# Optimization experiments

Measured on AMD Instinct MI355X. Metric: run time of the kernel, lower is better.

## Reference

```python
import jax, jax.numpy as jnp
import numpy as np

EPS = 1e-5  # torch BatchNorm1d default eps


def _bn(x, gamma, beta):
    # training-mode BatchNorm1d over the point dimension
    m = jnp.mean(x, axis=0)
    v = jnp.var(x, axis=0)
    return (x - m) * jax.lax.rsqrt(v + EPS) * gamma + beta


def setup_inputs() -> dict:
    key = jax.random.key(0)
    ks = jax.random.split(key, 8)
    N, D = 1000000, 9
    G, V = 32, 32768  # 32^3 voxel grid; with 1M points all voxels occupied w.h.p.
    feats = jax.random.normal(ks[0], (N, D), dtype=jnp.float32)
    coords = jax.random.randint(ks[1], (N, 3), 0, G, dtype=jnp.int32)

    def lin(k, fan_in, fan_out):
        kw, kb = jax.random.split(k)
        s = 1.0 / np.sqrt(fan_in)
        W = jax.random.uniform(kw, (fan_in, fan_out), jnp.float32, -s, s)
        b = jax.random.uniform(kb, (fan_out,), jnp.float32, -s, s)
        return W, b

    W1, b1 = lin(ks[2], 9, 64)
    W2, b2 = lin(ks[3], 64, 128)
    W3, b3 = lin(ks[4], 128, 256)
    W4, b4 = lin(ks[5], 256, 256)
    return {
        'feats': feats, 'coords': coords, 'num_voxels': V,
        'g0': jnp.ones((9,), jnp.float32), 'be0': jnp.zeros((9,), jnp.float32),
        'W1': W1, 'b1': b1,
        'g1': jnp.ones((64,), jnp.float32), 'be1': jnp.zeros((64,), jnp.float32),
        'W2': W2, 'b2': b2,
        'g2': jnp.ones((128,), jnp.float32), 'be2': jnp.zeros((128,), jnp.float32),
        'W3': W3, 'b3': b3,
        'g3': jnp.ones((256,), jnp.float32), 'be3': jnp.zeros((256,), jnp.float32),
        'W4': W4, 'b4': b4,
    }


def _mlp(x, g0, be0, W1, b1, g1, be1, W2, b2, g2, be2, W3, b3, g3, be3, W4, b4):
    x = _bn(x, g0, be0)
    x = jax.nn.relu(_bn(x @ W1 + b1, g1, be1))
    x = jax.nn.relu(_bn(x @ W2 + b2, g2, be2))
    x = jax.nn.relu(_bn(x @ W3 + b3, g3, be3))
    return x @ W4 + b4


def reference(feats, coords, num_voxels, g0, be0, W1, b1, g1, be1, W2, b2,
              g2, be2, W3, b3, g3, be3, W4, b4):
    # NOTE: the torch module shuffles points first; unique(dim=0) is sorted and
    # scatter_max is permutation-invariant, so the shuffle does not affect output.
    unq_coords, unq_inv = jnp.unique(
        coords, axis=0, return_inverse=True, size=num_voxels, fill_value=0)
    unq_inv = unq_inv.reshape(-1)
    unq_coords = unq_coords.astype(jnp.int64)
    h = _mlp(feats, g0, be0, W1, b1, g1, be1, W2, b2, g2, be2, W3, b3, g3, be3, W4, b4)
    pooled = jax.ops.segment_max(h, unq_inv, num_segments=num_voxels)  # [V, 256]
    return pooled, unq_coords
```

## Files before the change

### kernel.cpp

```cpp
#include <hip/hip_runtime.h>
#include <math.h>

#define TPB 256
#define PT 64
#define NVOX 32768
#define VB 8
#define BN_EPS 1e-5f

typedef short s16x8 __attribute__((ext_vector_type(8)));
typedef short s16x4 __attribute__((ext_vector_type(4)));
typedef float f32x4 __attribute__((ext_vector_type(4)));

#define P0_OFF     0u
#define P1_OFF     256u
#define P2_OFF     (P1_OFF + 64u*128u*4u)
#define P3_OFF     (P2_OFF + 64u*256u*4u)
#define PAR_END    (P3_OFF + 64u*512u*4u)
#define A0_OFF     229632u
#define C0_OFF     229888u
#define A1_OFF     230144u
#define C1_OFF     230400u
#define A2_OFF     230656u
#define C2_OFF     231680u
#define A3_OFF     232704u
#define C3_OFF     233728u
#define HIST_OFF   234752u
#define BASE_OFF   (HIST_OFF + 131072u)
#define CURS_OFF   (BASE_OFF + 131328u)
#define PERM_OFF   (CURS_OFF + 131072u)
#define WT1_OFF    (PERM_OFF + 4000000u)
#define WT2_OFF    (WT1_OFF + 4096u)
#define WT3_OFF    (WT2_OFF + 16384u)
#define WT4_OFF    (WT3_OFF + 65536u)
#define X_OFF      4845568u

#define ACT0_OFF 0
#define ACT1_OFF 4096
#define ACT2_OFF 12288
#define ACT3_OFF 32768
#define H4_OFF   0
#define SMEM_S1  4096
#define SMEM_S2  12288
#define SMEM_S3  28672
#define SMEM_S4  65536

__device__ __forceinline__ unsigned short f2bf(float f) {
    unsigned u = __float_as_uint(f);
    u += 0x7FFFu + ((u >> 16) & 1u);
    return (unsigned short)(u >> 16);
}
__device__ __forceinline__ float bf2f(unsigned short h) {
    return __uint_as_float(((unsigned)h) << 16);
}

template<int ROWB>
__device__ __forceinline__ int swz(int row, int b) {
    constexpr int M = (ROWB >= 128) ? 7 : ((ROWB >= 64) ? 3 : 1);
    return row * ROWB + (b ^ ((row & M) << 4));
}

__device__ __forceinline__ s16x4 bn_relu_pack(f32x4 acc, f32x4 av, f32x4 cv) {
    s16x4 pk;
#pragma unroll
    for (int r = 0; r < 4; ++r) pk[r] = (short)f2bf(fmaxf(fmaf(acc[r], av[r], cv[r]), 0.f));
    return pk;
}

template<int NOUT>
__device__ __forceinline__ void stats_red(f32x4 ps, f32x4 pq, int ch, float* prow) {
#pragma unroll
    for (int m = 1; m <= 8; m <<= 1) {
#pragma unroll
        for (int r = 0; r < 4; ++r) { ps[r] += __shfl_xor(ps[r], m); pq[r] += __shfl_xor(pq[r], m); }
    }
    if ((threadIdx.x & 15) == 0) {
#pragma unroll
        for (int r = 0; r < 4; ++r) {
            atomicAdd(&prow[ch + r], ps[r]);
            atomicAdd(&prow[NOUT + ch + r], pq[r]);
        }
    }
}

__global__ void k_prepw(const float* __restrict__ W1, const float* __restrict__ W2,
                        const float* __restrict__ W3, const float* __restrict__ W4,
                        unsigned short* __restrict__ wt1, unsigned short* __restrict__ wt2,
                        unsigned short* __restrict__ wt3, unsigned short* __restrict__ wt4) {
    for (int i = blockIdx.x * blockDim.x + threadIdx.x; i < 108544;
         i += gridDim.x * blockDim.x) {
        if (i < 2048) {
            int n = i >> 5, k = i & 31;
            wt1[i] = (k < 9) ? f2bf(W1[k * 64 + n]) : (unsigned short)0;
        } else if (i < 10240) {
            int j = i - 2048; int n = j >> 6, k = j & 63;
            wt2[j] = f2bf(W2[k * 128 + n]);
        } else if (i < 43008) {
            int j = i - 10240; int n = j >> 7, k = j & 127;
            wt3[j] = f2bf(W3[k * 256 + n]);
        } else {
            int j = i - 43008; int n = j >> 8, k = j & 255;
            wt4[j] = f2bf(W4[k * 256 + n]);
        }
    }
}

__global__ void k_hist(const int* __restrict__ coords, int N, unsigned* __restrict__ hist) {
    for (int i = blockIdx.x * blockDim.x + threadIdx.x; i < N;
         i += gridDim.x * blockDim.x) {
        int v = (coords[3 * i] << 10) | (coords[3 * i + 1] << 5) | coords[3 * i + 2];
        atomicAdd(&hist[v], 1u);
    }
}

__global__ void k_scan(const unsigned* __restrict__ hist, int* __restrict__ base,
                       unsigned* __restrict__ cursor, int N) {
    __shared__ unsigned part[1024];
    const int t = threadIdx.x;
    unsigned sum = 0;
    for (int j = 0; j < 32; ++j) sum += hist[t * 32 + j];
    part[t] = sum;
    __syncthreads();
    for (int d = 1; d < 1024; d <<= 1) {
        unsigned v = (t >= d) ? part[t - d] : 0u;
        __syncthreads();
        part[t] += v;
        __syncthreads();
    }
    unsigned run = part[t] - sum;
    for (int j = 0; j < 32; ++j) {
        unsigned h = hist[t * 32 + j];
        base[t * 32 + j] = (int)run;
        cursor[t * 32 + j] = run;
        run += h;
    }
    if (t == 1023) base[32768] = (int)run;
}

__global__ void k_scatter(const int* __restrict__ coords, int N,
                          unsigned* __restrict__ cursor, int* __restrict__ perm) {
    for (int i = blockIdx.x * blockDim.x + threadIdx.x; i < N;
         i += gridDim.x * blockDim.x) {
        int v = (coords[3 * i] << 10) | (coords[3 * i + 1] << 5) | coords[3 * i + 2];
        unsigned pos = atomicAdd(&cursor[v], 1u);
        perm[pos] = i;
    }
}

__global__ void k_stats0(const float* __restrict__ feats, int N, float* __restrict__ p0) {
    __shared__ float s[9], q[9];
    if (threadIdx.x < 9) { s[threadIdx.x] = 0.f; q[threadIdx.x] = 0.f; }
    __syncthreads();
    float ls[9] = {0}, lq[9] = {0};
    for (size_t i = (size_t)blockIdx.x * blockDim.x + threadIdx.x; i < (size_t)N;
         i += (size_t)gridDim.x * blockDim.x) {
        const float* r = feats + i * 9;
#pragma unroll
        for (int c = 0; c < 9; ++c) { float v = r[c]; ls[c] += v; lq[c] += v * v; }
    }
#pragma unroll
    for (int c = 0; c < 9; ++c) { atomicAdd(&s[c], ls[c]); atomicAdd(&q[c], lq[c]); }
    __syncthreads();
    if (threadIdx.x < 9) {
        atomicAdd(&p0[threadIdx.x], s[threadIdx.x]);
        atomicAdd(&p0[9 + threadIdx.x], q[threadIdx.x]);
    }
}

__global__ void k_fin(const float* __restrict__ part, int nparts, int C,
                      const float* __restrict__ g, const float* __restrict__ be,
                      const float* __restrict__ bias,
                      float* __restrict__ A, float* __restrict__ Cc, float n) {
    int c = threadIdx.x;
    if (c >= C) return;
    float s = 0.f, q = 0.f;
    for (int r = 0; r < nparts; ++r) { s += part[r * 2 * C + c]; q += part[r * 2 * C + C + c]; }
    float m = s / n;
    float v = q / n - m * m;
    float a = g[c] * rsqrtf(v + BN_EPS);
    float cc = be[c] - m * a;
    A[c] = a;
    Cc[c] = bias ? fmaf(a, bias[c], cc) : cc;
}

__global__ void k_coords(float* __restrict__ outc) {
    int v = blockIdx.x * blockDim.x + threadIdx.x;
    if (v < NVOX) {
        outc[3 * v + 0] = (float)(v >> 10);
        outc[3 * v + 1] = (float)((v >> 5) & 31);
        outc[3 * v + 2] = (float)(v & 31);
    }
}


__global__ __launch_bounds__(256, 4) void k_pass1(
    const float* __restrict__ feats, const int* __restrict__ perm,
    const unsigned short* __restrict__ wt1,
    const float* __restrict__ A0, const float* __restrict__ C0,
    const float* __restrict__ b1,
    unsigned short* __restrict__ Xg, float* __restrict__ p1,
    int N, int nt) {
    __shared__ char Xl[8192];
    const int tid = threadIdx.x;
    const int w = tid >> 6, lane = tid & 63, g = lane >> 4, lq = lane & 15;
    const int chb = w * 16;
    const s16x8 a1 = *(const s16x8*)(wt1 + (chb + lq) * 32 + g * 8);
    const int ch = chb + g * 4;
    const f32x4 bv = *(const f32x4*)(b1 + ch);
    float* prow = p1 + (blockIdx.x & 63) * 128;

    for (int t = blockIdx.x; t < nt; t += gridDim.x) {
        const int t0 = t * 128;
        *(f32x4*)(Xl + tid * 32) = (f32x4){0.f, 0.f, 0.f, 0.f};
        *(f32x4*)(Xl + tid * 32 + 16) = (f32x4){0.f, 0.f, 0.f, 0.f};
        __syncthreads();
        for (int idx = tid; idx < 128 * 9; idx += 256) {
            const int p = idx / 9, c = idx - p * 9;
            const int gp = t0 + p;
            if (gp < N) {
                const int src = perm[gp];
                float v = fmaf(feats[(size_t)src * 9 + c], A0[c], C0[c]);
                *(unsigned short*)(Xl + swz<64>(p, c * 2)) = f2bf(v);
            }
        }
        __syncthreads();
        {
            const int row = tid >> 1, c = (tid & 1) * 16;
            *(s16x8*)(Xg + (size_t)(t0 + row) * 16 + c / 2) =
                *(const s16x8*)(Xl + swz<64>(row, c));
        }
        f32x4 acc[8];
#pragma unroll
        for (int ct = 0; ct < 8; ++ct) acc[ct] = (f32x4){0.f, 0.f, 0.f, 0.f};
#pragma unroll
        for (int ct = 0; ct < 8; ++ct) {
            const s16x8 b = *(const s16x8*)(Xl + swz<64>(ct * 16 + lq, g * 16));
            acc[ct] = __builtin_amdgcn_mfma_f32_16x16x32_bf16(a1, b, acc[ct], 0, 0, 0);
        }
        f32x4 ps = (f32x4){0.f,0.f,0.f,0.f}, pq = (f32x4){0.f,0.f,0.f,0.f};
#pragma unroll
        for (int ct = 0; ct < 8; ++ct) {
            const bool valid = (t0 + ct * 16 + lq) < N;
#pragma unroll
            for (int r = 0; r < 4; ++r) {
                const float h = valid ? (acc[ct][r] + bv[r]) : 0.f;
                ps[r] += h; pq[r] += h * h;
            }
        }
        stats_red<64>(ps, pq, ch, prow);
        __syncthreads();
    }
}

__global__ __launch_bounds__(256, 2) void k_pass2(
    const unsigned short* __restrict__ Xg,
    const unsigned short* __restrict__ wt1, const unsigned short* __restrict__ wt2,
    const float* __restrict__ A1, const float* __restrict__ C1,
    const float* __restrict__ b2,
    float* __restrict__ p2, int N, int nt) {
    __shared__ char smem[40960];
    char* Wt2l = smem;
    char* Xl   = smem + 16384;
    char* act1 = smem + 24576;
    const int tid = threadIdx.x;
    const int w = tid >> 6, lane = tid & 63, g = lane >> 4, lq = lane & 15;
    const int chb1 = w * 16, chb2 = w * 32;

    for (int i = tid; i < 1024; i += 256) {
        const int row = i >> 3, c = (i & 7) * 16;
        *(s16x8*)(Wt2l + swz<128>(row, c)) = *(const s16x8*)(wt2 + row * 64 + c / 2);
    }
    const s16x8 a1 = *(const s16x8*)(wt1 + (chb1 + lq) * 32 + g * 8);
    const int ch1 = chb1 + g * 4;
    const f32x4 av1 = *(const f32x4*)(A1 + ch1);
    const f32x4 cv1 = *(const f32x4*)(C1 + ch1);
    f32x4 bv2[2];
#pragma unroll
    for (int mt = 0; mt < 2; ++mt) bv2[mt] = *(const f32x4*)(b2 + chb2 + mt * 16 + g * 4);
    float* prow = p2 + (blockIdx.x & 63) * 256;

    for (int t = blockIdx.x; t < nt; t += gridDim.x) {
        const int t0 = t * 128;
        for (int i = tid; i < 512; i += 256) {
            const int row = i >> 2, c = (i & 3) * 16;
            s16x8 v = (s16x8){0,0,0,0,0,0,0,0};
            if (c < 32) v = *(const s16x8*)(Xg + (size_t)(t0 + row) * 16 + c / 2);
            *(s16x8*)(Xl + swz<64>(row, c)) = v;
        }
        __syncthreads();
        f32x4 acc1[8];
#pragma unroll
        for (int ct = 0; ct < 8; ++ct) acc1[ct] = (f32x4){0.f,0.f,0.f,0.f};
#pragma unroll
        for (int ct = 0; ct < 8; ++ct) {
            const s16x8 b = *(const s16x8*)(Xl + swz<64>(ct * 16 + lq, g * 16));
            acc1[ct] = __builtin_amdgcn_mfma_f32_16x16x32_bf16(a1, b, acc1[ct], 0, 0, 0);
        }
#pragma unroll
        for (int ct = 0; ct < 8; ++ct)
            *(s16x4*)(act1 + swz<128>(ct * 16 + lq, ch1 * 2)) = bn_relu_pack(acc1[ct], av1, cv1);
        __syncthreads();
        f32x4 acc2[2][8];
#pragma unroll
        for (int mt = 0; mt < 2; ++mt)
#pragma unroll
            for (int ct = 0; ct < 8; ++ct) acc2[mt][ct] = (f32x4){0.f,0.f,0.f,0.f};
#pragma unroll
        for (int kc = 0; kc < 2; ++kc) {
            s16x8 a[2];
#pragma unroll
            for (int mt = 0; mt < 2; ++mt)
                a[mt] = *(const s16x8*)(Wt2l + swz<128>(chb2 + mt * 16 + lq, kc * 64 + g * 16));
#pragma unroll
            for (int ct = 0; ct < 8; ++ct) {
                const s16x8 b = *(const s16x8*)(act1 + swz<128>(ct * 16 + lq, kc * 64 + g * 16));
#pragma unroll
                for (int mt = 0; mt < 2; ++mt)
                    acc2[mt][ct] = __builtin_amdgcn_mfma_f32_16x16x32_bf16(a[mt], b, acc2[mt][ct], 0, 0, 0);
            }
        }
#pragma unroll
        for (int mt = 0; mt < 2; ++mt) {
            f32x4 ps = (f32x4){0.f,0.f,0.f,0.f}, pq = (f32x4){0.f,0.f,0.f,0.f};
#pragma unroll
            for (int ct = 0; ct < 8; ++ct) {
                const bool valid = (t0 + ct * 16 + lq) < N;
#pragma unroll
                for (int r = 0; r < 4; ++r) {
                    const float h = valid ? (acc2[mt][ct][r] + bv2[mt][r]) : 0.f;
                    ps[r] += h; pq[r] += h * h;
                }
            }
            stats_red<128>(ps, pq, chb2 + mt * 16 + g * 4, prow);
        }
        __syncthreads();
    }
}

__global__ __launch_bounds__(512, 2) void k_pass3(
    const unsigned short* __restrict__ Xg,
    const unsigned short* __restrict__ wt1, const unsigned short* __restrict__ wt2,
    const unsigned short* __restrict__ wt3,
    const float* __restrict__ A1, const float* __restrict__ C1,
    const float* __restrict__ A2, const float* __restrict__ C2,
    const float* __restrict__ b3,
    float* __restrict__ p3, int N, int nt) {
    extern __shared__ char smem[];
    char* Wt2l = smem;
    char* act1 = smem + 16384;
    char* act2 = smem + 32768;
    char* Xl   = smem + 32768;
    const int tid = threadIdx.x;
    const int w = tid >> 6, lane = tid & 63, g = lane >> 4, lq = lane & 15;
    const int wm = w >> 1, wn = w & 1;
    const int chb1 = wm * 16, chb2 = w * 16, chb3 = w * 32;

    for (int i = tid; i < 1024; i += 512) {
        const int row = i >> 3, c = (i & 7) * 16;
        *(s16x8*)(Wt2l + swz<128>(row, c)) = *(const s16x8*)(wt2 + row * 64 + c / 2);
    }
    s16x8 w3[2][4];
#pragma unroll
    for (int mt = 0; mt < 2; ++mt)
#pragma unroll
        for (int kc = 0; kc < 4; ++kc)
            w3[mt][kc] = *(const s16x8*)(wt3 + (size_t)(chb3 + mt * 16 + lq) * 128 + kc * 32 + g * 8);
    const s16x8 a1 = *(const s16x8*)(wt1 + (chb1 + lq) * 32 + g * 8);
    const int ch1 = chb1 + g * 4, ch2 = chb2 + g * 4;
    const f32x4 av1 = *(const f32x4*)(A1 + ch1);
    const f32x4 cv1 = *(const f32x4*)(C1 + ch1);
    const f32x4 av2 = *(const f32x4*)(A2 + ch2);
    const f32x4 cv2 = *(const f32x4*)(C2 + ch2);
    f32x4 bv3[2];
#pragma unroll
    for (int mt = 0; mt < 2; ++mt) bv3[mt] = *(const f32x4*)(b3 + chb3 + mt * 16 + g * 4);
    float* prow = p3 + (blockIdx.x & 63) * 512;

    for (int t = blockIdx.x; t < nt; t += gridDim.x) {
        const int t0 = t * 128;
        {
            const int row = tid >> 2, c = (tid & 3) * 16;
            s16x8 v = (s16x8){0,0,0,0,0,0,0,0};
            if (c < 32) v = *(const s16x8*)(Xg + (size_t)(t0 + row) * 16 + c / 2);
            *(s16x8*)(Xl + swz<64>(row, c)) = v;
        }
        __syncthreads();
        f32x4 acc1[4];
#pragma unroll
        for (int ct = 0; ct < 4; ++ct) acc1[ct] = (f32x4){0.f,0.f,0.f,0.f};
#pragma unroll
        for (int ct = 0; ct < 4; ++ct) {
            const int row = wn * 64 + ct * 16 + lq;
            const s16x8 b = *(const s16x8*)(Xl + swz<64>(row, g * 16));
            acc1[ct] = __builtin_amdgcn_mfma_f32_16x16x32_bf16(a1, b, acc1[ct], 0, 0, 0);
        }
#pragma unroll
        for (int ct = 0; ct < 4; ++ct) {
            const int row = wn * 64 + ct * 16 + lq;
            *(s16x4*)(act1 + swz<128>(row, ch1 * 2)) = bn_relu_pack(acc1[ct], av1, cv1);
        }
        __syncthreads();
        f32x4 acc2[8];
#pragma unroll
        for (int ct = 0; ct < 8; ++ct) acc2[ct] = (f32x4){0.f,0.f,0.f,0.f};
#pragma unroll
        for (int kc = 0; kc < 2; ++kc) {
            const s16x8 a = *(const s16x8*)(Wt2l + swz<128>(chb2 + lq, kc * 64 + g * 16));
#pragma unroll
            for (int ct = 0; ct < 8; ++ct) {
                const s16x8 b = *(const s16x8*)(act1 + swz<128>(ct * 16 + lq, kc * 64 + g * 16));
                acc2[ct] = __builtin_amdgcn_mfma_f32_16x16x32_bf16(a, b, acc2[ct], 0, 0, 0);
            }
        }
#pragma unroll
        for (int ct = 0; ct < 8; ++ct)
            *(s16x4*)(act2 + swz<256>(ct * 16 + lq, ch2 * 2)) = bn_relu_pack(acc2[ct], av2, cv2);
        __syncthreads();
        f32x4 acc3[2][8];
#pragma unroll
        for (int mt = 0; mt < 2; ++mt)
#pragma unroll
            for (int ct = 0; ct < 8; ++ct) acc3[mt][ct] = (f32x4){0.f,0.f,0.f,0.f};
#pragma unroll
        for (int kc = 0; kc < 4; ++kc) {
#pragma unroll
            for (int ct = 0; ct < 8; ++ct) {
                const s16x8 b = *(const s16x8*)(act2 + swz<256>(ct * 16 + lq, kc * 64 + g * 16));
#pragma unroll
                for (int mt = 0; mt < 2; ++mt)
                    acc3[mt][ct] = __builtin_amdgcn_mfma_f32_16x16x32_bf16(w3[mt][kc], b, acc3[mt][ct], 0, 0, 0);
            }
        }
#pragma unroll
        for (int mt = 0; mt < 2; ++mt) {
            f32x4 ps = (f32x4){0.f,0.f,0.f,0.f}, pq = (f32x4){0.f,0.f,0.f,0.f};
#pragma unroll
            for (int ct = 0; ct < 8; ++ct) {
                const bool valid = (t0 + ct * 16 + lq) < N;
#pragma unroll
                for (int r = 0; r < 4; ++r) {
                    const float h = valid ? (acc3[mt][ct][r] + bv3[mt][r]) : 0.f;
                    ps[r] += h; pq[r] += h * h;
                }
            }
            stats_red<256>(ps, pq, chb3 + mt * 16 + g * 4, prow);
        }
        __syncthreads();
    }
}

__global__ __launch_bounds__(512, 2) void k_pass4(
    const unsigned short* __restrict__ Xg,
    const unsigned short* __restrict__ wt1, const unsigned short* __restrict__ wt2,
    const unsigned short* __restrict__ wt3, const unsigned short* __restrict__ wt4,
    const float* __restrict__ A1, const float* __restrict__ C1,
    const float* __restrict__ A2, const float* __restrict__ C2,
    const float* __restrict__ A3, const float* __restrict__ C3,
    const float* __restrict__ b4,
    const int* __restrict__ base, float* __restrict__ out) {
    extern __shared__ char smem[];
    char* Wt2l = smem;
    char* act1 = smem + 16384;
    char* H    = smem + 24576;
    char* act3 = smem + 57344;
    char* Xl   = smem + 57344;
    const int tid = threadIdx.x;
    const int w = tid >> 6, lane = tid & 63, g = lane >> 4, lq = lane & 15;
    const int wm = w >> 1, wn = w & 1;
    const int chb1 = wm * 16, chb2 = w * 16, chb = w * 32;

    for (int i = tid; i < 1024; i += 512) {
        const int row = i >> 3, c = (i & 7) * 16;
        *(s16x8*)(Wt2l + swz<128>(row, c)) = *(const s16x8*)(wt2 + row * 64 + c / 2);
    }
    s16x8 w3[2][4], w4[2][8];
#pragma unroll
    for (int mt = 0; mt < 2; ++mt) {
#pragma unroll
        for (int kc = 0; kc < 4; ++kc)
            w3[mt][kc] = *(const s16x8*)(wt3 + (size_t)(chb + mt * 16 + lq) * 128 + kc * 32 + g * 8);
#pragma unroll
        for (int kc = 0; kc < 8; ++kc)
            w4[mt][kc] = *(const s16x8*)(wt4 + (size_t)(chb + mt * 16 + lq) * 256 + kc * 32 + g * 8);
    }
    const s16x8 a1 = *(const s16x8*)(wt1 + (chb1 + lq) * 32 + g * 8);
    const int ch1 = chb1 + g * 4, ch2 = chb2 + g * 4;
    const f32x4 av1 = *(const f32x4*)(A1 + ch1);
    const f32x4 cv1 = *(const f32x4*)(C1 + ch1);
    const f32x4 av2 = *(const f32x4*)(A2 + ch2);
    const f32x4 cv2 = *(const f32x4*)(C2 + ch2);
    f32x4 av3[2], cv3[2], bv4[2];
#pragma unroll
    for (int mt = 0; mt < 2; ++mt) {
        av3[mt] = *(const f32x4*)(A3 + chb + mt * 16 + g * 4);
        cv3[mt] = *(const f32x4*)(C3 + chb + mt * 16 + g * 4);
        bv4[mt] = *(const f32x4*)(b4 + chb + mt * 16 + g * 4);
    }

    const int vb = blockIdx.x * 16;
    const int pstart = base[vb], pend = base[vb + 16];
    const int chgrp = tid & 31, slot = tid >> 5;
    const int vlo = base[vb + slot], vhi = base[vb + slot + 1];
    float rmax[8];
#pragma unroll
    for (int j = 0; j < 8; ++j) rmax[j] = -INFINITY;

    for (int t0 = pstart; t0 < pend; t0 += 64) {
        if (tid < 256) {
            const int row = tid >> 2, c = (tid & 3) * 16;
            const int gp = t0 + row;
            s16x8 v = (s16x8){0,0,0,0,0,0,0,0};
            if (c < 32 && gp < pend) v = *(const s16x8*)(Xg + (size_t)gp * 16 + c / 2);
            *(s16x8*)(Xl + swz<64>(row, c)) = v;
        }
        __syncthreads();
        f32x4 acc1[2];
#pragma unroll
        for (int ct = 0; ct < 2; ++ct) acc1[ct] = (f32x4){0.f,0.f,0.f,0.f};
#pragma unroll
        for (int ct = 0; ct < 2; ++ct) {
            const int row = wn * 32 + ct * 16 + lq;
            const s16x8 b = *(const s16x8*)(Xl + swz<64>(row, g * 16));
            acc1[ct] = __builtin_amdgcn_mfma_f32_16x16x32_bf16(a1, b, acc1[ct], 0, 0, 0);
        }
#pragma unroll
        for (int ct = 0; ct < 2; ++ct) {
            const int row = wn * 32 + ct * 16 + lq;
            *(s16x4*)(act1 + swz<128>(row, ch1 * 2)) = bn_relu_pack(acc1[ct], av1, cv1);
        }
        __syncthreads();
        f32x4 acc2[4];
#pragma unroll
        for (int ct = 0; ct < 4; ++ct) acc2[ct] = (f32x4){0.f,0.f,0.f,0.f};
#pragma unroll
        for (int kc = 0; kc < 2; ++kc) {
            const s16x8 a = *(const s16x8*)(Wt2l + swz<128>(chb2 + lq, kc * 64 + g * 16));
#pragma unroll
            for (int ct = 0; ct < 4; ++ct) {
                const s16x8 b = *(const s16x8*)(act1 + swz<128>(ct * 16 + lq, kc * 64 + g * 16));
                acc2[ct] = __builtin_amdgcn_mfma_f32_16x16x32_bf16(a, b, acc2[ct], 0, 0, 0);
            }
        }
#pragma unroll
        for (int ct = 0; ct < 4; ++ct)
            *(s16x4*)(H + swz<256>(ct * 16 + lq, ch2 * 2)) = bn_relu_pack(acc2[ct], av2, cv2);
        __syncthreads();
        f32x4 acc3[2][4];
#pragma unroll
        for (int mt = 0; mt < 2; ++mt)
#pragma unroll
            for (int ct = 0; ct < 4; ++ct) acc3[mt][ct] = (f32x4){0.f,0.f,0.f,0.f};
#pragma unroll
        for (int kc = 0; kc < 4; ++kc) {
#pragma unroll
            for (int ct = 0; ct < 4; ++ct) {
                const s16x8 b = *(const s16x8*)(H + swz<256>(ct * 16 + lq, kc * 64 + g * 16));
#pragma unroll
                for (int mt = 0; mt < 2; ++mt)
                    acc3[mt][ct] = __builtin_amdgcn_mfma_f32_16x16x32_bf16(w3[mt][kc], b, acc3[mt][ct], 0, 0, 0);
            }
        }
#pragma unroll
        for (int mt = 0; mt < 2; ++mt)
#pragma unroll
            for (int ct = 0; ct < 4; ++ct)
                *(s16x4*)(act3 + swz<512>(ct * 16 + lq, (chb + mt * 16 + g * 4) * 2)) =
                    bn_relu_pack(acc3[mt][ct], av3[mt], cv3[mt]);
        __syncthreads();
        f32x4 acc4[2][4];
#pragma unroll
        for (int mt = 0; mt < 2; ++mt)
#pragma unroll
            for (int ct = 0; ct < 4; ++ct) acc4[mt][ct] = (f32x4){0.f,0.f,0.f,0.f};
#pragma unroll
        for (int kc = 0; kc < 8; ++kc) {
#pragma unroll
            for (int ct = 0; ct < 4; ++ct) {
                const s16x8 b = *(const s16x8*)(act3 + swz<512>(ct * 16 + lq, kc * 64 + g * 16));
#pragma unroll
                for (int mt = 0; mt < 2; ++mt)
                    acc4[mt][ct] = __builtin_amdgcn_mfma_f32_16x16x32_bf16(w4[mt][kc], b, acc4[mt][ct], 0, 0, 0);
            }
        }
#pragma unroll
        for (int mt = 0; mt < 2; ++mt) {
#pragma unroll
            for (int ct = 0; ct < 4; ++ct) {
                s16x4 pk;
#pragma unroll
                for (int r = 0; r < 4; ++r) pk[r] = (short)f2bf(acc4[mt][ct][r] + bv4[mt][r]);
                *(s16x4*)(H + swz<512>(ct * 16 + lq, (chb + mt * 16 + g * 4) * 2)) = pk;
            }
        }
        __syncthreads();
        {
            const int lo = max(vlo, t0), hi = min(vhi, t0 + 64);
            for (int p = lo; p < hi; ++p) {
                const s16x8 hv = *(const s16x8*)(H + swz<512>(p - t0, chgrp * 16));
#pragma unroll
                for (int j = 0; j < 8; ++j)
                    rmax[j] = fmaxf(rmax[j], bf2f((unsigned short)hv[j]));
            }
        }
        __syncthreads();
    }
    float* orow = out + (size_t)(vb + slot) * 256 + chgrp * 8;
    f32x4 o0, o1;
#pragma unroll
    for (int j = 0; j < 4; ++j) { o0[j] = rmax[j]; o1[j] = rmax[4 + j]; }
    *(f32x4*)orow = o0;
    *(f32x4*)(orow + 4) = o1;
}

template<int NOUT, int K, int MODE>
__device__ __forceinline__ void layer(
    const unsigned short* __restrict__ wt,
    const char* __restrict__ lds_in, char* __restrict__ lds_out,
    const float* __restrict__ Af, const float* __restrict__ Cf,
    const float* __restrict__ bias, float* __restrict__ part,
    int p0, int N, int tid) {
    constexpr int ROWB_IN = K * 2;
    constexpr int ROWB_OUT = NOUT * 2;
    constexpr int MT = NOUT / 64;
    constexpr int KC = K / 32;
    const int w = tid >> 6, lane = tid & 63, g = lane >> 4, lq = lane & 15;
    const int chbase = w * (NOUT / 4);

    f32x4 acc[MT][4];
#pragma unroll
    for (int mt = 0; mt < MT; ++mt)
#pragma unroll
        for (int ct = 0; ct < 4; ++ct) acc[mt][ct] = (f32x4){0.f, 0.f, 0.f, 0.f};

#pragma unroll
    for (int kc = 0; kc < KC; ++kc) {
        s16x8 a[MT];
#pragma unroll
        for (int mt = 0; mt < MT; ++mt)
            a[mt] = *(const s16x8*)(wt + (size_t)(chbase + mt * 16 + lq) * K + kc * 32 + g * 8);
#pragma unroll
        for (int ct = 0; ct < 4; ++ct) {
            const int row = ct * 16 + lq;
            s16x8 b = *(const s16x8*)(lds_in + swz<ROWB_IN>(row, kc * 64 + g * 16));
#pragma unroll
            for (int mt = 0; mt < MT; ++mt)
                acc[mt][ct] = __builtin_amdgcn_mfma_f32_16x16x32_bf16(a[mt], b, acc[mt][ct], 0, 0, 0);
        }
    }

    if constexpr (MODE == 0) {
#pragma unroll
        for (int mt = 0; mt < MT; ++mt) {
            const int ch = chbase + mt * 16 + g * 4;
            const f32x4 av = *(const f32x4*)(Af + ch);
            const f32x4 cv = *(const f32x4*)(Cf + ch);
#pragma unroll
            for (int ct = 0; ct < 4; ++ct) {
                const int row = ct * 16 + lq;
                *(s16x4*)(lds_out + swz<ROWB_OUT>(row, ch * 2)) = bn_relu_pack(acc[mt][ct], av, cv);
            }
        }
    } else if constexpr (MODE == 1) {
#pragma unroll
        for (int mt = 0; mt < MT; ++mt) {
            const int ch = chbase + mt * 16 + g * 4;
            const f32x4 bv = *(const f32x4*)(bias + ch);
            f32x4 ps = (f32x4){0.f, 0.f, 0.f, 0.f}, pq = (f32x4){0.f, 0.f, 0.f, 0.f};
#pragma unroll
            for (int ct = 0; ct < 4; ++ct) {
                const bool valid = (p0 + ct * 16 + lq) < N;
#pragma unroll
                for (int r = 0; r < 4; ++r) {
                    float h = valid ? (acc[mt][ct][r] + bv[r]) : 0.f;
                    ps[r] += h; pq[r] += h * h;
                }
            }
            stats_red<NOUT>(ps, pq, ch, part);
        }
    } else {
#pragma unroll
        for (int mt = 0; mt < MT; ++mt) {
            const int ch = chbase + mt * 16 + g * 4;
            const f32x4 bv = *(const f32x4*)(bias + ch);
#pragma unroll
            for (int ct = 0; ct < 4; ++ct) {
                const int row = ct * 16 + lq;
                s16x4 pk;
#pragma unroll
                for (int r = 0; r < 4; ++r)
                    pk[r] = (short)f2bf(acc[mt][ct][r] + bv[r]);
                *(s16x4*)(lds_out + swz<ROWB_OUT>(row, ch * 2)) = pk;
            }
        }
    }
}

__device__ __forceinline__ void stage_act0(const float* __restrict__ feats,
                                           const float* __restrict__ A0,
                                           const float* __restrict__ C0,
                                           const int* __restrict__ perm,
                                           int t0, int pend, char* act0, int tid) {
    *(f32x4*)(act0 + tid * 16) = (f32x4){0.f, 0.f, 0.f, 0.f};
    __syncthreads();
    for (int idx = tid; idx < PT * 9; idx += TPB) {
        const int p = idx / 9, ch = idx - p * 9;
        const int gp = t0 + p;
        if (gp < pend) {
            const int src = perm ? perm[gp] : gp;
            float v = fmaf(feats[(size_t)src * 9 + ch], A0[ch], C0[ch]);
            *(unsigned short*)(act0 + swz<64>(p, ch * 2)) = f2bf(v);
        }
    }
}

template<int STAGE>
__global__ __launch_bounds__(TPB, 2) void k_stage(
    const float* __restrict__ feats, char* __restrict__ ws,
    const float* __restrict__ b1, const float* __restrict__ b2,
    const float* __restrict__ b3, const float* __restrict__ b4,
    float* __restrict__ out, int N) {
    extern __shared__ char smem[];
    char* act0 = smem + ACT0_OFF;
    char* act1 = smem + ACT1_OFF;
    char* act2 = smem + ACT2_OFF;
    char* act3 = smem + ACT3_OFF;
    char* h4   = smem + H4_OFF;

    const int tid = threadIdx.x;
    const float* A0 = (const float*)(ws + A0_OFF);
    const float* C0 = (const float*)(ws + C0_OFF);
    const float* A1 = (const float*)(ws + A1_OFF);
    const float* C1 = (const float*)(ws + C1_OFF);
    const float* A2 = (const float*)(ws + A2_OFF);
    const float* C2 = (const float*)(ws + C2_OFF);
    const float* A3 = (const float*)(ws + A3_OFF);
    const float* C3 = (const float*)(ws + C3_OFF);
    const unsigned short* Wt1 = (const unsigned short*)(ws + WT1_OFF);
    const unsigned short* Wt2 = (const unsigned short*)(ws + WT2_OFF);
    const unsigned short* Wt3 = (const unsigned short*)(ws + WT3_OFF);
    const unsigned short* Wt4 = (const unsigned short*)(ws + WT4_OFF);

    if constexpr (STAGE < 4) {
        const int t0 = blockIdx.x * PT;
        stage_act0(feats, A0, C0, nullptr, t0, N, act0, tid);
        __syncthreads();
        if constexpr (STAGE == 1) {
            float* prow = (float*)(ws + P1_OFF) + (blockIdx.x & 63) * 128;
            layer<64, 32, 1>(Wt1, act0, nullptr, nullptr, nullptr, b1, prow, t0, N, tid);
            return;
        }
        layer<64, 32, 0>(Wt1, act0, act1, A1, C1, nullptr, nullptr, t0, N, tid);
        __syncthreads();
        if constexpr (STAGE == 2) {
            float* prow = (float*)(ws + P2_OFF) + (blockIdx.x & 63) * 256;
            layer<128, 64, 1>(Wt2, act1, nullptr, nullptr, nullptr, b2, prow, t0, N, tid);
            return;
        }
        layer<128, 64, 0>(Wt2, act1, act2, A2, C2, nullptr, nullptr, t0, N, tid);
        __syncthreads();
        float* prow = (float*)(ws + P3_OFF) + (blockIdx.x & 63) * 512;
        layer<256, 128, 1>(Wt3, act2, nullptr, nullptr, nullptr, b3, prow, t0, N, tid);
    } else {
        const int* base = (const int*)(ws + BASE_OFF);
        const int* perm = (const int*)(ws + PERM_OFF);
        const int vb = blockIdx.x * VB;
        const int pstart = base[vb], pend = base[vb + VB];
        const int chgrp = tid & 31, slot = tid >> 5;
        const int vlo = base[vb + slot], vhi = base[vb + slot + 1];
        float rmax[8];
#pragma unroll
        for (int j = 0; j < 8; ++j) rmax[j] = -INFINITY;

        for (int t0 = pstart; t0 < pend; t0 += PT) {
            stage_act0(feats, A0, C0, perm, t0, pend, act0, tid);
            __syncthreads();
            layer<64, 32, 0>(Wt1, act0, act1, A1, C1, nullptr, nullptr, t0, N, tid);
            __syncthreads();
            layer<128, 64, 0>(Wt2, act1, act2, A2, C2, nullptr, nullptr, t0, N, tid);
            __syncthreads();
            layer<256, 128, 0>(Wt3, act2, act3, A3, C3, nullptr, nullptr, t0, N, tid);
            __syncthreads();
            layer<256, 256, 2>(Wt4, act3, h4, nullptr, nullptr, b4, nullptr, t0, N, tid);
            __syncthreads();
            const int lo = max(vlo, t0), hi = min(vhi, t0 + PT);
            for (int p = lo; p < hi; ++p) {
                const int row = p - t0;
                s16x8 hv = *(const s16x8*)(h4 + swz<512>(row, chgrp * 16));
#pragma unroll
                for (int j = 0; j < 8; ++j)
                    rmax[j] = fmaxf(rmax[j], bf2f((unsigned short)hv[j]));
            }
            __syncthreads();
        }
        float* orow = out + (size_t)(vb + slot) * 256 + chgrp * 8;
        f32x4 o0, o1;
#pragma unroll
        for (int j = 0; j < 4; ++j) { o0[j] = rmax[j]; o1[j] = rmax[4 + j]; }
        *(f32x4*)orow = o0;
        *(f32x4*)(orow + 4) = o1;
    }
}

extern "C" void kernel_launch(void* const* d_in, const int* in_sizes, int n_in,
                              void* d_out, int out_size, void* d_ws, size_t ws_size,
                              hipStream_t stream) {
    const float* feats = (const float*)d_in[0];
    const int* coords = (const int*)d_in[1];
    const float* g0 = (const float*)d_in[3];
    const float* be0 = (const float*)d_in[4];
    const float* W1 = (const float*)d_in[5];
    const float* b1 = (const float*)d_in[6];
    const float* g1 = (const float*)d_in[7];
    const float* be1 = (const float*)d_in[8];
    const float* W2 = (const float*)d_in[9];
    const float* b2 = (const float*)d_in[10];
    const float* g2 = (const float*)d_in[11];
    const float* be2 = (const float*)d_in[12];
    const float* W3 = (const float*)d_in[13];
    const float* b3 = (const float*)d_in[14];
    const float* g3 = (const float*)d_in[15];
    const float* be3 = (const float*)d_in[16];
    const float* W4 = (const float*)d_in[17];
    const float* b4 = (const float*)d_in[18];
    float* out = (float*)d_out;
    char* ws = (char*)d_ws;

    const int N = in_sizes[0] / 9;
    const float fN = (float)N;
    const int nt = (N + 127) / 128;

    hipMemsetAsync(ws, 0, PAR_END, stream);
    hipMemsetAsync(ws + HIST_OFF, 0, 131072, stream);

    k_prepw<<<128, TPB, 0, stream>>>(W1, W2, W3, W4,
        (unsigned short*)(ws + WT1_OFF), (unsigned short*)(ws + WT2_OFF),
        (unsigned short*)(ws + WT3_OFF), (unsigned short*)(ws + WT4_OFF));
    k_hist<<<1024, TPB, 0, stream>>>(coords, N, (unsigned*)(ws + HIST_OFF));
    k_scan<<<1, 1024, 0, stream>>>((const unsigned*)(ws + HIST_OFF),
                                   (int*)(ws + BASE_OFF), (unsigned*)(ws + CURS_OFF), N);
    k_scatter<<<1024, TPB, 0, stream>>>(coords, N, (unsigned*)(ws + CURS_OFF),
                                        (int*)(ws + PERM_OFF));

    k_stats0<<<256, TPB, 0, stream>>>(feats, N, (float*)(ws + P0_OFF));
    k_fin<<<1, TPB, 0, stream>>>((const float*)(ws + P0_OFF), 1, 9, g0, be0, nullptr,
                                 (float*)(ws + A0_OFF), (float*)(ws + C0_OFF), fN);
    k_coords<<<(NVOX + TPB - 1) / TPB, TPB, 0, stream>>>(out + (size_t)NVOX * 256);

    const size_t need = (size_t)X_OFF + (size_t)nt * 4096u;
    if (ws_size >= need && N <= 1000000) {
        unsigned short* Xg = (unsigned short*)(ws + X_OFF);
        const unsigned short* wt1 = (const unsigned short*)(ws + WT1_OFF);
        const unsigned short* wt2 = (const unsigned short*)(ws + WT2_OFF);
        const unsigned short* wt3 = (const unsigned short*)(ws + WT3_OFF);
        const unsigned short* wt4 = (const unsigned short*)(ws + WT4_OFF);
        const float* A0 = (const float*)(ws + A0_OFF);
        const float* C0 = (const float*)(ws + C0_OFF);
        float* A1 = (float*)(ws + A1_OFF); float* C1 = (float*)(ws + C1_OFF);
        float* A2 = (float*)(ws + A2_OFF); float* C2 = (float*)(ws + C2_OFF);
        float* A3 = (float*)(ws + A3_OFF); float* C3 = (float*)(ws + C3_OFF);

        hipFuncSetAttribute((const void*)k_pass3,
            hipFuncAttributeMaxDynamicSharedMemorySize, 65536);
        hipFuncSetAttribute((const void*)k_pass4,
            hipFuncAttributeMaxDynamicSharedMemorySize, 90112);

        k_pass1<<<1024, 256, 0, stream>>>(feats, (const int*)(ws + PERM_OFF), wt1,
            A0, C0, b1, Xg, (float*)(ws + P1_OFF), N, nt);
        k_fin<<<1, TPB, 0, stream>>>((const float*)(ws + P1_OFF), 64, 64, g1, be1, b1,
                                     A1, C1, fN);
        k_pass2<<<1024, 256, 0, stream>>>(Xg, wt1, wt2, A1, C1, b2,
                                          (float*)(ws + P2_OFF), N, nt);
        k_fin<<<1, TPB, 0, stream>>>((const float*)(ws + P2_OFF), 64, 128, g2, be2, b2,
                                     A2, C2, fN);
        k_pass3<<<1024, 512, 65536, stream>>>(Xg, wt1, wt2, wt3, A1, C1, A2, C2, b3,
                                              (float*)(ws + P3_OFF), N, nt);
        k_fin<<<1, TPB, 0, stream>>>((const float*)(ws + P3_OFF), 64, 256, g3, be3, b3,
                                     A3, C3, fN);
        k_pass4<<<NVOX / 16, 512, 90112, stream>>>(Xg, wt1, wt2, wt3, wt4,
            A1, C1, A2, C2, A3, C3, b4, (const int*)(ws + BASE_OFF), out);
    } else {
        const int nblk = (N + PT - 1) / PT;
        k_stage<1><<<nblk, TPB, SMEM_S1, stream>>>(feats, ws, b1, b2, b3, b4, out, N);
        k_fin<<<1, TPB, 0, stream>>>((const float*)(ws + P1_OFF), 64, 64, g1, be1, b1,
                                     (float*)(ws + A1_OFF), (float*)(ws + C1_OFF), fN);
        k_stage<2><<<nblk, TPB, SMEM_S2, stream>>>(feats, ws, b1, b2, b3, b4, out, N);
        k_fin<<<1, TPB, 0, stream>>>((const float*)(ws + P2_OFF), 64, 128, g2, be2, b2,
                                     (float*)(ws + A2_OFF), (float*)(ws + C2_OFF), fN);
        k_stage<3><<<nblk, TPB, SMEM_S3, stream>>>(feats, ws, b1, b2, b3, b4, out, N);
        k_fin<<<1, TPB, 0, stream>>>((const float*)(ws + P3_OFF), 64, 256, g3, be3, b3,
                                     (float*)(ws + A3_OFF), (float*)(ws + C3_OFF), fN);
        k_stage<4><<<NVOX / VB, TPB, SMEM_S4, stream>>>(feats, ws, b1, b2, b3, b4, out, N);
    }
}
```

Before: 1.014 ms.

## Materialize layer-3 activations to avoid recompute in pooling pass; trim LDS staging

Pass 3 can now write its pre-BN layer-3 outputs as bf16 to a global buffer. A new pooling kernel then applies BN/ReLU and only the final matmul, instead of recomputing layers 1-3 per voxel. Separately, the W2 tiles and the input tiles are read straight from global into registers rather than staged through LDS, and the histogram and input-stats kernels are fused into one. This trades a large extra global write and read (about 512 MB of bf16) for removing the recompute, and drops the old fallback path.

After: 1.010 ms. Within noise of the previous version (-0.4%).

```diff
diff --git a/kernel.cpp b/kernel.cpp
--- a/kernel.cpp
+++ b/kernel.cpp
@@ -2,9 +2,7 @@
 #include <math.h>
 
 #define TPB 256
-#define PT 64
 #define NVOX 32768
-#define VB 8
 #define BN_EPS 1e-5f
 
 typedef short s16x8 __attribute__((ext_vector_type(8)));
@@ -34,16 +32,6 @@
 #define WT4_OFF    (WT3_OFF + 65536u)
 #define X_OFF      4845568u
 
-#define ACT0_OFF 0
-#define ACT1_OFF 4096
-#define ACT2_OFF 12288
-#define ACT3_OFF 32768
-#define H4_OFF   0
-#define SMEM_S1  4096
-#define SMEM_S2  12288
-#define SMEM_S3  28672
-#define SMEM_S4  65536
-
 __device__ __forceinline__ unsigned short f2bf(float f) {
     unsigned u = __float_as_uint(f);
     u += 0x7FFFu + ((u >> 16) & 1u);
@@ -104,11 +92,26 @@
     }
 }
 
-__global__ void k_hist(const int* __restrict__ coords, int N, unsigned* __restrict__ hist) {
+__global__ void k_hist_stats(const int* __restrict__ coords, const float* __restrict__ feats,
+                             int N, unsigned* __restrict__ hist, float* __restrict__ p0) {
+    __shared__ float s[9], q[9];
+    if (threadIdx.x < 9) { s[threadIdx.x] = 0.f; q[threadIdx.x] = 0.f; }
+    __syncthreads();
+    float ls[9] = {0}, lq[9] = {0};
     for (int i = blockIdx.x * blockDim.x + threadIdx.x; i < N;
          i += gridDim.x * blockDim.x) {
         int v = (coords[3 * i] << 10) | (coords[3 * i + 1] << 5) | coords[3 * i + 2];
         atomicAdd(&hist[v], 1u);
+        const float* r = feats + (size_t)i * 9;
+#pragma unroll
+        for (int c = 0; c < 9; ++c) { float x = r[c]; ls[c] += x; lq[c] += x * x; }
+    }
+#pragma unroll
+    for (int c = 0; c < 9; ++c) { atomicAdd(&s[c], ls[c]); atomicAdd(&q[c], lq[c]); }
+    __syncthreads();
+    if (threadIdx.x < 9) {
+        atomicAdd(&p0[threadIdx.x], s[threadIdx.x]);
+        atomicAdd(&p0[9 + threadIdx.x], q[threadIdx.x]);
     }
 }
 
@@ -143,26 +146,6 @@
         int v = (coords[3 * i] << 10) | (coords[3 * i + 1] << 5) | coords[3 * i + 2];
         unsigned pos = atomicAdd(&cursor[v], 1u);
         perm[pos] = i;
-    }
-}
-
-__global__ void k_stats0(const float* __restrict__ feats, int N, float* __restrict__ p0) {
-    __shared__ float s[9], q[9];
-    if (threadIdx.x < 9) { s[threadIdx.x] = 0.f; q[threadIdx.x] = 0.f; }
-    __syncthreads();
-    float ls[9] = {0}, lq[9] = {0};
-    for (size_t i = (size_t)blockIdx.x * blockDim.x + threadIdx.x; i < (size_t)N;
-         i += (size_t)gridDim.x * blockDim.x) {
-        const float* r = feats + i * 9;
-#pragma unroll
-        for (int c = 0; c < 9; ++c) { float v = r[c]; ls[c] += v; lq[c] += v * v; }
-    }
-#pragma unroll
-    for (int c = 0; c < 9; ++c) { atomicAdd(&s[c], ls[c]); atomicAdd(&q[c], lq[c]); }
-    __syncthreads();
-    if (threadIdx.x < 9) {
-        atomicAdd(&p0[threadIdx.x], s[threadIdx.x]);
-        atomicAdd(&p0[9 + threadIdx.x], q[threadIdx.x]);
     }
 }
 
@@ -190,7 +173,6 @@
         outc[3 * v + 2] = (float)(v & 31);
     }
 }
-
 
 __global__ __launch_bounds__(256, 4) void k_pass1(
     const float* __restrict__ feats, const int* __restrict__ perm,
@@ -251,25 +233,24 @@
     }
 }
 
-__global__ __launch_bounds__(256, 2) void k_pass2(
+__global__ __launch_bounds__(256) void k_pass2(
     const unsigned short* __restrict__ Xg,
     const unsigned short* __restrict__ wt1, const unsigned short* __restrict__ wt2,
     const float* __restrict__ A1, const float* __restrict__ C1,
     const float* __restrict__ b2,
     float* __restrict__ p2, int N, int nt) {
-    __shared__ char smem[40960];
-    char* Wt2l = smem;
-    char* Xl   = smem + 16384;
-    char* act1 = smem + 24576;
+    __shared__ char act1[16384];
     const int tid = threadIdx.x;
     const int w = tid >> 6, lane = tid & 63, g = lane >> 4, lq = lane & 15;
     const int chb1 = w * 16, chb2 = w * 32;
 
-    for (int i = tid; i < 1024; i += 256) {
-        const int row = i >> 3, c = (i & 7) * 16;
-        *(s16x8*)(Wt2l + swz<128>(row, c)) = *(const s16x8*)(wt2 + row * 64 + c / 2);
-    }
     const s16x8 a1 = *(const s16x8*)(wt1 + (chb1 + lq) * 32 + g * 8);
+    s16x8 w2f[2][2];
+#pragma unroll
+    for (int mt = 0; mt < 2; ++mt)
+#pragma unroll
+        for (int kc = 0; kc < 2; ++kc)
+            w2f[mt][kc] = *(const s16x8*)(wt2 + (size_t)(chb2 + mt * 16 + lq) * 64 + kc * 32 + g * 8);
     const int ch1 = chb1 + g * 4;
     const f32x4 av1 = *(const f32x4*)(A1 + ch1);
     const f32x4 cv1 = *(const f32x4*)(C1 + ch1);
@@ -280,25 +261,19 @@
 
     for (int t = blockIdx.x; t < nt; t += gridDim.x) {
         const int t0 = t * 128;
-        for (int i = tid; i < 512; i += 256) {
-            const int row = i >> 2, c = (i & 3) * 16;
-            s16x8 v = (s16x8){0,0,0,0,0,0,0,0};
-            if (c < 32) v = *(const s16x8*)(Xg + (size_t)(t0 + row) * 16 + c / 2);
-            *(s16x8*)(Xl + swz<64>(row, c)) = v;
-        }
-        __syncthreads();
         f32x4 acc1[8];
 #pragma unroll
         for (int ct = 0; ct < 8; ++ct) acc1[ct] = (f32x4){0.f,0.f,0.f,0.f};
 #pragma unroll
         for (int ct = 0; ct < 8; ++ct) {
-            const s16x8 b = *(const s16x8*)(Xl + swz<64>(ct * 16 + lq, g * 16));
+            const s16x8 b = *(const s16x8*)(Xg + (size_t)(t0 + ct * 16 + lq) * 16 + g * 8);
             acc1[ct] = __builtin_amdgcn_mfma_f32_16x16x32_bf16(a1, b, acc1[ct], 0, 0, 0);
         }
 #pragma unroll
         for (int ct = 0; ct < 8; ++ct)
             *(s16x4*)(act1 + swz<128>(ct * 16 + lq, ch1 * 2)) = bn_relu_pack(acc1[ct], av1, cv1);
         __syncthreads();
+
         f32x4 acc2[2][8];
 #pragma unroll
         for (int mt = 0; mt < 2; ++mt)
@@ -306,16 +281,12 @@
             for (int ct = 0; ct < 8; ++ct) acc2[mt][ct] = (f32x4){0.f,0.f,0.f,0.f};
 #pragma unroll
         for (int kc = 0; kc < 2; ++kc) {
-            s16x8 a[2];
-#pragma unroll
-            for (int mt = 0; mt < 2; ++mt)
-                a[mt] = *(const s16x8*)(Wt2l + swz<128>(chb2 + mt * 16 + lq, kc * 64 + g * 16));
 #pragma unroll
             for (int ct = 0; ct < 8; ++ct) {
                 const s16x8 b = *(const s16x8*)(act1 + swz<128>(ct * 16 + lq, kc * 64 + g * 16));
 #pragma unroll
                 for (int mt = 0; mt < 2; ++mt)
-                    acc2[mt][ct] = __builtin_amdgcn_mfma_f32_16x16x32_bf16(a[mt], b, acc2[mt][ct], 0, 0, 0);
+                    acc2[mt][ct] = __builtin_amdgcn_mfma_f32_16x16x32_bf16(w2f[mt][kc], b, acc2[mt][ct], 0, 0, 0);
             }
         }
 #pragma unroll
@@ -336,35 +307,33 @@
     }
 }
 
-__global__ __launch_bounds__(512, 2) void k_pass3(
+template<int DUMP>
+__global__ __launch_bounds__(512) void k_pass3(
     const unsigned short* __restrict__ Xg,
     const unsigned short* __restrict__ wt1, const unsigned short* __restrict__ wt2,
     const unsigned short* __restrict__ wt3,
     const float* __restrict__ A1, const float* __restrict__ C1,
     const float* __restrict__ A2, const float* __restrict__ C2,
     const float* __restrict__ b3,
-    float* __restrict__ p3, int N, int nt) {
-    extern __shared__ char smem[];
-    char* Wt2l = smem;
-    char* act1 = smem + 16384;
-    char* act2 = smem + 32768;
-    char* Xl   = smem + 32768;
+    float* __restrict__ p3, unsigned short* __restrict__ h3g,
+    int N, int nt) {
+    __shared__ char act1[16384];
+    __shared__ char act2[32768];
     const int tid = threadIdx.x;
     const int w = tid >> 6, lane = tid & 63, g = lane >> 4, lq = lane & 15;
     const int wm = w >> 1, wn = w & 1;
     const int chb1 = wm * 16, chb2 = w * 16, chb3 = w * 32;
 
-    for (int i = tid; i < 1024; i += 512) {
-        const int row = i >> 3, c = (i & 7) * 16;
-        *(s16x8*)(Wt2l + swz<128>(row, c)) = *(const s16x8*)(wt2 + row * 64 + c / 2);
-    }
-    s16x8 w3[2][4];
+    const s16x8 a1 = *(const s16x8*)(wt1 + (chb1 + lq) * 32 + g * 8);
+    s16x8 w2f[2], w3f[2][4];
+#pragma unroll
+    for (int kc = 0; kc < 2; ++kc)
+        w2f[kc] = *(const s16x8*)(wt2 + (size_t)(chb2 + lq) * 64 + kc * 32 + g * 8);
 #pragma unroll
     for (int mt = 0; mt < 2; ++mt)
 #pragma unroll
         for (int kc = 0; kc < 4; ++kc)
-            w3[mt][kc] = *(const s16x8*)(wt3 + (size_t)(chb3 + mt * 16 + lq) * 128 + kc * 32 + g * 8);
-    const s16x8 a1 = *(const s16x8*)(wt1 + (chb1 + lq) * 32 + g * 8);
+            w3f[mt][kc] = *(const s16x8*)(wt3 + (size_t)(chb3 + mt * 16 + lq) * 128 + kc * 32 + g * 8);
     const int ch1 = chb1 + g * 4, ch2 = chb2 + g * 4;
     const f32x4 av1 = *(const f32x4*)(A1 + ch1);
     const f32x4 cv1 = *(const f32x4*)(C1 + ch1);
@@ -377,20 +346,13 @@
 
     for (int t = blockIdx.x; t < nt; t += gridDim.x) {
         const int t0 = t * 128;
-        {
-            const int row = tid >> 2, c = (tid & 3) * 16;
-            s16x8 v = (s16x8){0,0,0,0,0,0,0,0};
-            if (c < 32) v = *(const s16x8*)(Xg + (size_t)(t0 + row) * 16 + c / 2);
-            *(s16x8*)(Xl + swz<64>(row, c)) = v;
-        }
-        __syncthreads();
         f32x4 acc1[4];
 #pragma unroll
         for (int ct = 0; ct < 4; ++ct) acc1[ct] = (f32x4){0.f,0.f,0.f,0.f};
 #pragma unroll
         for (int ct = 0; ct < 4; ++ct) {
             const int row = wn * 64 + ct * 16 + lq;
-            const s16x8 b = *(const s16x8*)(Xl + swz<64>(row, g * 16));
+            const s16x8 b = *(const s16x8*)(Xg + (size_t)(t0 + row) * 16 + g * 8);
             acc1[ct] = __builtin_amdgcn_mfma_f32_16x16x32_bf16(a1, b, acc1[ct], 0, 0, 0);
         }
 #pragma unroll
@@ -404,11 +366,10 @@
         for (int ct = 0; ct < 8; ++ct) acc2[ct] = (f32x4){0.f,0.f,0.f,0.f};
 #pragma unroll
         for (int kc = 0; kc < 2; ++kc) {
-            const s16x8 a = *(const s16x8*)(Wt2l + swz<128>(chb2 + lq, kc * 64 + g * 16));
 #pragma unroll
             for (int ct = 0; ct < 8; ++ct) {
                 const s16x8 b = *(const s16x8*)(act1 + swz<128>(ct * 16 + lq, kc * 64 + g * 16));
-                acc2[ct] = __builtin_amdgcn_mfma_f32_16x16x32_bf16(a, b, acc2[ct], 0, 0, 0);
+                acc2[ct] = __builtin_amdgcn_mfma_f32_16x16x32_bf16(w2f[kc], b, acc2[ct], 0, 0, 0);
             }
         }
 #pragma unroll
@@ -427,7 +388,23 @@
                 const s16x8 b = *(const s16x8*)(act2 + swz<256>(ct * 16 + lq, kc * 64 + g * 16));
 #pragma unroll
                 for (int mt = 0; mt < 2; ++mt)
-                    acc3[mt][ct] = __builtin_amdgcn_mfma_f32_16x16x32_bf16(w3[mt][kc], b, acc3[mt][ct], 0, 0, 0);
+                    acc3[mt][ct] = __builtin_amdgcn_mfma_f32_16x16x32_bf16(w3f[mt][kc], b, acc3[mt][ct], 0, 0, 0);
+            }
+        }
+        if constexpr (DUMP) {
+#pragma unroll
+            for (int mt = 0; mt < 2; ++mt) {
+                const int ch = chb3 + mt * 16 + g * 4;
+#pragma unroll
+                for (int ct = 0; ct < 8; ++ct) {
+                    const int pt = t0 + ct * 16 + lq;
+                    if (pt < N) {
+                        s16x4 pk;
+#pragma unroll
+                        for (int r = 0; r < 4; ++r) pk[r] = (short)f2bf(acc3[mt][ct][r]);
+                        *(s16x4*)(h3g + (size_t)pt * 256 + ch) = pk;
+                    }
+                }
             }
         }
 #pragma unroll
@@ -448,7 +425,7 @@
     }
 }
 
-__global__ __launch_bounds__(512, 2) void k_pass4(
+__global__ __launch_bounds__(512) void k_pass4(
     const unsigned short* __restrict__ Xg,
     const unsigned short* __restrict__ wt1, const unsigned short* __restrict__ wt2,
     const unsigned short* __restrict__ wt3, const unsigned short* __restrict__ wt4,
@@ -458,21 +435,19 @@
     const float* __restrict__ b4,
     const int* __restrict__ base, float* __restrict__ out) {
     extern __shared__ char smem[];
-    char* Wt2l = smem;
-    char* act1 = smem + 16384;
-    char* H    = smem + 24576;
-    char* act3 = smem + 57344;
-    char* Xl   = smem + 57344;
+    char* act1 = smem;
+    char* H    = smem + 8192;
+    char* act3 = smem + 40960;
     const int tid = threadIdx.x;
     const int w = tid >> 6, lane = tid & 63, g = lane >> 4, lq = lane & 15;
     const int wm = w >> 1, wn = w & 1;
     const int chb1 = wm * 16, chb2 = w * 16, chb = w * 32;
 
-    for (int i = tid; i < 1024; i += 512) {
-        const int row = i >> 3, c = (i & 7) * 16;
-        *(s16x8*)(Wt2l + swz<128>(row, c)) = *(const s16x8*)(wt2 + row * 64 + c / 2);
-    }
-    s16x8 w3[2][4], w4[2][8];
+    const s16x8 a1 = *(const s16x8*)(wt1 + (chb1 + lq) * 32 + g * 8);
+    s16x8 w2f[2], w3[2][4], w4[2][8];
+#pragma unroll
+    for (int kc = 0; kc < 2; ++kc)
+        w2f[kc] = *(const s16x8*)(wt2 + (size_t)(chb2 + lq) * 64 + kc * 32 + g * 8);
 #pragma unroll
     for (int mt = 0; mt < 2; ++mt) {
 #pragma unroll
@@ -482,7 +457,6 @@
         for (int kc = 0; kc < 8; ++kc)
             w4[mt][kc] = *(const s16x8*)(wt4 + (size_t)(chb + mt * 16 + lq) * 256 + kc * 32 + g * 8);
     }
-    const s16x8 a1 = *(const s16x8*)(wt1 + (chb1 + lq) * 32 + g * 8);
     const int ch1 = chb1 + g * 4, ch2 = chb2 + g * 4;
     const f32x4 av1 = *(const f32x4*)(A1 + ch1);
     const f32x4 cv1 = *(const f32x4*)(C1 + ch1);
@@ -505,21 +479,13 @@
     for (int j = 0; j < 8; ++j) rmax[j] = -INFINITY;
 
     for (int t0 = pstart; t0 < pend; t0 += 64) {
-        if (tid < 256) {
-            const int row = tid >> 2, c = (tid & 3) * 16;
-            const int gp = t0 + row;
-            s16x8 v = (s16x8){0,0,0,0,0,0,0,0};
-            if (c < 32 && gp < pend) v = *(const s16x8*)(Xg + (size_t)gp * 16 + c / 2);
-            *(s16x8*)(Xl + swz<64>(row, c)) = v;
-        }
-        __syncthreads();
         f32x4 acc1[2];
 #pragma unroll
         for (int ct = 0; ct < 2; ++ct) acc1[ct] = (f32x4){0.f,0.f,0.f,0.f};
 #pragma unroll
         for (int ct = 0; ct < 2; ++ct) {
             const int row = wn * 32 + ct * 16 + lq;
-            const s16x8 b = *(const s16x8*)(Xl + swz<64>(row, g * 16));
+            const s16x8 b = *(const s16x8*)(Xg + (size_t)(t0 + row) * 16 + g * 8);
             acc1[ct] = __builtin_amdgcn_mfma_f32_16x16x32_bf16(a1, b, acc1[ct], 0, 0, 0);
         }
 #pragma unroll
@@ -533,11 +499,10 @@
         for (int ct = 0; ct < 4; ++ct) acc2[ct] = (f32x4){0.f,0.f,0.f,0.f};
 #pragma unroll
         for (int kc = 0; kc < 2; ++kc) {
-            const s16x8 a = *(const s16x8*)(Wt2l + swz<128>(chb2 + lq, kc * 64 + g * 16));
 #pragma unroll
             for (int ct = 0; ct < 4; ++ct) {
                 const s16x8 b = *(const s16x8*)(act1 + swz<128>(ct * 16 + lq, kc * 64 + g * 16));
-                acc2[ct] = __builtin_amdgcn_mfma_f32_16x16x32_bf16(a, b, acc2[ct], 0, 0, 0);
+                acc2[ct] = __builtin_amdgcn_mfma_f32_16x16x32_bf16(w2f[kc], b, acc2[ct], 0, 0, 0);
             }
         }
 #pragma unroll
@@ -611,193 +576,102 @@
     *(f32x4*)(orow + 4) = o1;
 }
 
-template<int NOUT, int K, int MODE>
-__device__ __forceinline__ void layer(
-    const unsigned short* __restrict__ wt,
-    const char* __restrict__ lds_in, char* __restrict__ lds_out,
-    const float* __restrict__ Af, const float* __restrict__ Cf,
-    const float* __restrict__ bias, float* __restrict__ part,
-    int p0, int N, int tid) {
-    constexpr int ROWB_IN = K * 2;
-    constexpr int ROWB_OUT = NOUT * 2;
-    constexpr int MT = NOUT / 64;
-    constexpr int KC = K / 32;
+__global__ __launch_bounds__(512) void k_pass4l(
+    const unsigned short* __restrict__ h3g,
+    const unsigned short* __restrict__ wt4,
+    const float* __restrict__ A3, const float* __restrict__ C3,
+    const float* __restrict__ b4,
+    const int* __restrict__ base, float* __restrict__ out, int N) {
+    extern __shared__ char smem[];
+    char* act3 = smem;
+    char* h4   = smem + 32768;
+    const int tid = threadIdx.x;
     const int w = tid >> 6, lane = tid & 63, g = lane >> 4, lq = lane & 15;
-    const int chbase = w * (NOUT / 4);
-
-    f32x4 acc[MT][4];
-#pragma unroll
-    for (int mt = 0; mt < MT; ++mt)
-#pragma unroll
-        for (int ct = 0; ct < 4; ++ct) acc[mt][ct] = (f32x4){0.f, 0.f, 0.f, 0.f};
-
-#pragma unroll
-    for (int kc = 0; kc < KC; ++kc) {
-        s16x8 a[MT];
-#pragma unroll
-        for (int mt = 0; mt < MT; ++mt)
-            a[mt] = *(const s16x8*)(wt + (size_t)(chbase + mt * 16 + lq) * K + kc * 32 + g * 8);
-#pragma unroll
-        for (int ct = 0; ct < 4; ++ct) {
-            const int row = ct * 16 + lq;
-            s16x8 b = *(const s16x8*)(lds_in + swz<ROWB_IN>(row, kc * 64 + g * 16));
-#pragma unroll
-            for (int mt = 0; mt < MT; ++mt)
-                acc[mt][ct] = __builtin_amdgcn_mfma_f32_16x16x32_bf16(a[mt], b, acc[mt][ct], 0, 0, 0);
-        }
-    }
-
-    if constexpr (MODE == 0) {
-#pragma unroll
-        for (int mt = 0; mt < MT; ++mt) {
-            const int ch = chbase + mt * 16 + g * 4;
-            const f32x4 av = *(const f32x4*)(Af + ch);
-            const f32x4 cv = *(const f32x4*)(Cf + ch);
+    const int chb = w * 32;
+
+    s16x8 w4f[2][8];
+#pragma unroll
+    for (int mt = 0; mt < 2; ++mt)
+#pragma unroll
+        for (int kc = 0; kc < 8; ++kc)
+            w4f[mt][kc] = *(const s16x8*)(wt4 + (size_t)(chb + mt * 16 + lq) * 256 + kc * 32 + g * 8);
+    f32x4 bv4[2];
+#pragma unroll
+    for (int mt = 0; mt < 2; ++mt) bv4[mt] = *(const f32x4*)(b4 + chb + mt * 16 + g * 4);
+
+    const int j = tid & 31, rowg = tid >> 5;
+    const int c8 = j * 8;
+    const f32x4 av3a = *(const f32x4*)(A3 + c8);
+    const f32x4 av3b = *(const f32x4*)(A3 + c8 + 4);
+    const f32x4 cv3a = *(const f32x4*)(C3 + c8);
+    const f32x4 cv3b = *(const f32x4*)(C3 + c8 + 4);
+
+    const int vb = blockIdx.x * 16;
+    const int pstart = base[vb], pend = base[vb + 16];
+    const int chgrp = tid & 31, slot = tid >> 5;
+    const int vlo = base[vb + slot], vhi = base[vb + slot + 1];
+    float rmax[8];
+#pragma unroll
+    for (int jj = 0; jj < 8; ++jj) rmax[jj] = -INFINITY;
+
+    for (int t0 = pstart; t0 < pend; t0 += 64) {
+#pragma unroll
+        for (int it = 0; it < 4; ++it) {
+            const int row = rowg + it * 16;
+            const int gp = min(t0 + row, N - 1);
+            const s16x8 v = *(const s16x8*)(h3g + (size_t)gp * 256 + c8);
+            s16x8 pk;
+#pragma unroll
+            for (int r = 0; r < 4; ++r) {
+                pk[r]     = (short)f2bf(fmaxf(fmaf(bf2f((unsigned short)v[r]), av3a[r], cv3a[r]), 0.f));
+                pk[4 + r] = (short)f2bf(fmaxf(fmaf(bf2f((unsigned short)v[4 + r]), av3b[r], cv3b[r]), 0.f));
+            }
+            *(s16x8*)(act3 + swz<512>(row, c8 * 2)) = pk;
+        }
+        __syncthreads();
+        f32x4 acc4[2][4];
+#pragma unroll
+        for (int mt = 0; mt < 2; ++mt)
+#pragma unroll
+            for (int ct = 0; ct < 4; ++ct) acc4[mt][ct] = (f32x4){0.f,0.f,0.f,0.f};
+#pragma unroll
+        for (int kc = 0; kc < 8; ++kc) {
 #pragma unroll
             for (int ct = 0; ct < 4; ++ct) {
-                const int row = ct * 16 + lq;
-                *(s16x4*)(lds_out + swz<ROWB_OUT>(row, ch * 2)) = bn_relu_pack(acc[mt][ct], av, cv);
-            }
-        }
-    } else if constexpr (MODE == 1) {
-#pragma unroll
-        for (int mt = 0; mt < MT; ++mt) {
-            const int ch = chbase + mt * 16 + g * 4;
-            const f32x4 bv = *(const f32x4*)(bias + ch);
-            f32x4 ps = (f32x4){0.f, 0.f, 0.f, 0.f}, pq = (f32x4){0.f, 0.f, 0.f, 0.f};
+                const s16x8 b = *(const s16x8*)(act3 + swz<512>(ct * 16 + lq, kc * 64 + g * 16));
+#pragma unroll
+                for (int mt = 0; mt < 2; ++mt)
+                    acc4[mt][ct] = __builtin_amdgcn_mfma_f32_16x16x32_bf16(w4f[mt][kc], b, acc4[mt][ct], 0, 0, 0);
+            }
+        }
+#pragma unroll
+        for (int mt = 0; mt < 2; ++mt) {
 #pragma unroll
             for (int ct = 0; ct < 4; ++ct) {
-                const bool valid = (p0 + ct * 16 + lq) < N;
-#pragma unroll
-                for (int r = 0; r < 4; ++r) {
-                    float h = valid ? (acc[mt][ct][r] + bv[r]) : 0.f;
-                    ps[r] += h; pq[r] += h * h;
-                }
-            }
-            stats_red<NOUT>(ps, pq, ch, part);
-        }
-    } else {
-#pragma unroll
-        for (int mt = 0; mt < MT; ++mt) {
-            const int ch = chbase + mt * 16 + g * 4;
-            const f32x4 bv = *(const f32x4*)(bias + ch);
-#pragma unroll
-            for (int ct = 0; ct < 4; ++ct) {
-                const int row = ct * 16 + lq;
                 s16x4 pk;
 #pragma unroll
-                for (int r = 0; r < 4; ++r)
-                    pk[r] = (short)f2bf(acc[mt][ct][r] + bv[r]);
-                *(s16x4*)(lds_out + swz<ROWB_OUT>(row, ch * 2)) = pk;
-            }
-        }
-    }
-}
-
-__device__ __forceinline__ void stage_act0(const float* __restrict__ feats,
-                                           const float* __restrict__ A0,
-                                           const float* __restrict__ C0,
-                                           const int* __restrict__ perm,
-                                           int t0, int pend, char* act0, int tid) {
-    *(f32x4*)(act0 + tid * 16) = (f32x4){0.f, 0.f, 0.f, 0.f};
-    __syncthreads();
-    for (int idx = tid; idx < PT * 9; idx += TPB) {
-        const int p = idx / 9, ch = idx - p * 9;
-        const int gp = t0 + p;
-        if (gp < pend) {
-            const int src = perm ? perm[gp] : gp;
-            float v = fmaf(feats[(size_t)src * 9 + ch], A0[ch], C0[ch]);
-            *(unsigned short*)(act0 + swz<64>(p, ch * 2)) = f2bf(v);
-        }
-    }
-}
-
-template<int STAGE>
-__global__ __launch_bounds__(TPB, 2) void k_stage(
-    const float* __restrict__ feats, char* __restrict__ ws,
-    const float* __restrict__ b1, const float* __restrict__ b2,
-    const float* __restrict__ b3, const float* __restrict__ b4,
-    float* __restrict__ out, int N) {
-    extern __shared__ char smem[];
-    char* act0 = smem + ACT0_OFF;
-    char* act1 = smem + ACT1_OFF;
-    char* act2 = smem + ACT2_OFF;
-    char* act3 = smem + ACT3_OFF;
-    char* h4   = smem + H4_OFF;
-
-    const int tid = threadIdx.x;
-    const float* A0 = (const float*)(ws + A0_OFF);
-    const float* C0 = (const float*)(ws + C0_OFF);
-    const float* A1 = (const float*)(ws + A1_OFF);
-    const float* C1 = (const float*)(ws + C1_OFF);
-    const float* A2 = (const float*)(ws + A2_OFF);
-    const float* C2 = (const float*)(ws + C2_OFF);
-    const float* A3 = (const float*)(ws + A3_OFF);
-    const float* C3 = (const float*)(ws + C3_OFF);
-    const unsigned short* Wt1 = (const unsigned short*)(ws + WT1_OFF);
-    const unsigned short* Wt2 = (const unsigned short*)(ws + WT2_OFF);
-    const unsigned short* Wt3 = (const unsigned short*)(ws + WT3_OFF);
-    const unsigned short* Wt4 = (const unsigned short*)(ws + WT4_OFF);
-
-    if constexpr (STAGE < 4) {
-        const int t0 = blockIdx.x * PT;
-        stage_act0(feats, A0, C0, nullptr, t0, N, act0, tid);
-        __syncthreads();
-        if constexpr (STAGE == 1) {
-            float* prow = (float*)(ws + P1_OFF) + (blockIdx.x & 63) * 128;
-            layer<64, 32, 1>(Wt1, act0, nullptr, nullptr, nullptr, b1, prow, t0, N, tid);
-            return;
-        }
-        layer<64, 32, 0>(Wt1, act0, act1, A1, C1, nullptr, nullptr, t0, N, tid);
-        __syncthreads();
-        if constexpr (STAGE == 2) {
-            float* prow = (float*)(ws + P2_OFF) + (blockIdx.x & 63) * 256;
-            layer<128, 64, 1>(Wt2, act1, nullptr, nullptr, nullptr, b2, prow, t0, N, tid);
-            return;
-        }
-        layer<128, 64, 0>(Wt2, act1, act2, A2, C2, nullptr, nullptr, t0, N, tid);
-        __syncthreads();
-        float* prow = (float*)(ws + P3_OFF) + (blockIdx.x & 63) * 512;
-        layer<256, 128, 1>(Wt3, act2, nullptr, nullptr, nullptr, b3, prow, t0, N, tid);
-    } else {
-        const int* base = (const int*)(ws + BASE_OFF);
-        const int* perm = (const int*)(ws + PERM_OFF);
-        const int vb = blockIdx.x * VB;
-        const int pstart = base[vb], pend = base[vb + VB];
-        const int chgrp = tid & 31, slot = tid >> 5;
-        const int vlo = base[vb + slot], vhi = base[vb + slot + 1];
-        float rmax[8];
-#pragma unroll
-        for (int j = 0; j < 8; ++j) rmax[j] = -INFINITY;
-
-        for (int t0 = pstart; t0 < pend; t0 += PT) {
-            stage_act0(feats, A0, C0, perm, t0, pend, act0, tid);
-            __syncthreads();
-            layer<64, 32, 0>(Wt1, act0, act1, A1, C1, nullptr, nullptr, t0, N, tid);
-            __syncthreads();
-            layer<128, 64, 0>(Wt2, act1, act2, A2, C2, nullptr, nullptr, t0, N, tid);
-            __syncthreads();
-            layer<256, 128, 0>(Wt3, act2, act3, A3, C3, nullptr, nullptr, t0, N, tid);
-            __syncthreads();
-            layer<256, 256, 2>(Wt4, act3, h4, nullptr, nullptr, b4, nullptr, t0, N, tid);
-            __syncthreads();
-            const int lo = max(vlo, t0), hi = min(vhi, t0 + PT);
+                for (int r = 0; r < 4; ++r) pk[r] = (short)f2bf(acc4[mt][ct][r] + bv4[mt][r]);
+                *(s16x4*)(h4 + swz<512>(ct * 16 + lq, (chb + mt * 16 + g * 4) * 2)) = pk;
+            }
+        }
+        __syncthreads();
+        {
+            const int lo = max(vlo, t0), hi = min(vhi, t0 + 64);
             for (int p = lo; p < hi; ++p) {
-                const int row = p - t0;
-                s16x8 hv = *(const s16x8*)(h4 + swz<512>(row, chgrp * 16));
-#pragma unroll
-                for (int j = 0; j < 8; ++j)
-                    rmax[j] = fmaxf(rmax[j], bf2f((unsigned short)hv[j]));
-            }
-            __syncthreads();
-        }
-        float* orow = out + (size_t)(vb + slot) * 256 + chgrp * 8;
-        f32x4 o0, o1;
-#pragma unroll
-        for (int j = 0; j < 4; ++j) { o0[j] = rmax[j]; o1[j] = rmax[4 + j]; }
-        *(f32x4*)orow = o0;
-        *(f32x4*)(orow + 4) = o1;
-    }
+                const s16x8 hv = *(const s16x8*)(h4 + swz<512>(p - t0, chgrp * 16));
+#pragma unroll
+                for (int jj = 0; jj < 8; ++jj)
+                    rmax[jj] = fmaxf(rmax[jj], bf2f((unsigned short)hv[jj]));
+            }
+        }
+        __syncthreads();
+    }
+    float* orow = out + (size_t)(vb + slot) * 256 + chgrp * 8;
+    f32x4 o0, o1;
+#pragma unroll
+    for (int jj = 0; jj < 4; ++jj) { o0[jj] = rmax[jj]; o1[jj] = rmax[4 + jj]; }
+    *(f32x4*)orow = o0;
+    *(f32x4*)(orow + 4) = o1;
 }
 
 extern "C" void kernel_launch(void* const* d_in, const int* in_sizes, int n_in,
@@ -828,66 +702,66 @@
     const float fN = (float)N;
     const int nt = (N + 127) / 128;
 
+    const size_t xg_bytes = (size_t)nt * 4096u + 8192u;
+    const size_t h3_off = X_OFF + ((xg_bytes + 255u) & ~(size_t)255u);
+    const size_t need_t2 = h3_off + (size_t)nt * 65536u + 65536u;
+    const bool t2 = (ws_size >= need_t2);
+
     hipMemsetAsync(ws, 0, PAR_END, stream);
     hipMemsetAsync(ws + HIST_OFF, 0, 131072, stream);
+
+    unsigned short* Xg = (unsigned short*)(ws + X_OFF);
+    unsigned short* H3 = (unsigned short*)(ws + h3_off);
+    const unsigned short* wt1 = (const unsigned short*)(ws + WT1_OFF);
+    const unsigned short* wt2 = (const unsigned short*)(ws + WT2_OFF);
+    const unsigned short* wt3 = (const unsigned short*)(ws + WT3_OFF);
+    const unsigned short* wt4 = (const unsigned short*)(ws + WT4_OFF);
+    float* A0 = (float*)(ws + A0_OFF); float* C0 = (float*)(ws + C0_OFF);
+    float* A1 = (float*)(ws + A1_OFF); float* C1 = (float*)(ws + C1_OFF);
+    float* A2 = (float*)(ws + A2_OFF); float* C2 = (float*)(ws + C2_OFF);
+    float* A3 = (float*)(ws + A3_OFF); float* C3 = (float*)(ws + C3_OFF);
+
+    hipFuncSetAttribute((const void*)k_pass4,
+        hipFuncAttributeMaxDynamicSharedMemorySize, 73728);
+    hipFuncSetAttribute((const void*)k_pass4l,
+        hipFuncAttributeMaxDynamicSharedMemorySize, 65536);
 
     k_prepw<<<128, TPB, 0, stream>>>(W1, W2, W3, W4,
         (unsigned short*)(ws + WT1_OFF), (unsigned short*)(ws + WT2_OFF),
         (unsigned short*)(ws + WT3_OFF), (unsigned short*)(ws + WT4_OFF));
-    k_hist<<<1024, TPB, 0, stream>>>(coords, N, (unsigned*)(ws + HIST_OFF));
+    k_hist_stats<<<1024, TPB, 0, stream>>>(coords, feats, N,
+        (unsigned*)(ws + HIST_OFF), (float*)(ws + P0_OFF));
     k_scan<<<1, 1024, 0, stream>>>((const unsigned*)(ws + HIST_OFF),
                                    (int*)(ws + BASE_OFF), (unsigned*)(ws + CURS_OFF), N);
     k_scatter<<<1024, TPB, 0, stream>>>(coords, N, (unsigned*)(ws + CURS_OFF),
                                         (int*)(ws + PERM_OFF));
-
-    k_stats0<<<256, TPB, 0, stream>>>(feats, N, (float*)(ws + P0_OFF));
     k_fin<<<1, TPB, 0, stream>>>((const float*)(ws + P0_OFF), 1, 9, g0, be0, nullptr,
-                                 (float*)(ws + A0_OFF), (float*)(ws + C0_OFF), fN);
+                                 A0, C0, fN);
     k_coords<<<(NVOX + TPB - 1) / TPB, TPB, 0, stream>>>(out + (size_t)NVOX * 256);
 
-    const size_t need = (size_t)X_OFF + (size_t)nt * 4096u;
-    if (ws_size >= need && N <= 1000000) {
-        unsigned short* Xg = (unsigned short*)(ws + X_OFF);
-        const unsigned short* wt1 = (const unsigned short*)(ws + WT1_OFF);
-        const unsigned short* wt2 = (const unsigned short*)(ws + WT2_OFF);
-        const unsigned short* wt3 = (const unsigned short*)(ws + WT3_OFF);
-        const unsigned short* wt4 = (const unsigned short*)(ws + WT4_OFF);
-        const float* A0 = (const float*)(ws + A0_OFF);
-        const float* C0 = (const float*)(ws + C0_OFF);
-        float* A1 = (float*)(ws + A1_OFF); float* C1 = (float*)(ws + C1_OFF);
-        float* A2 = (float*)(ws + A2_OFF); float* C2 = (float*)(ws + C2_OFF);
-        float* A3 = (float*)(ws + A3_OFF); float* C3 = (float*)(ws + C3_OFF);
-
-        hipFuncSetAttribute((const void*)k_pass3,
-            hipFuncAttributeMaxDynamicSharedMemorySize, 65536);
-        hipFuncSetAttribute((const void*)k_pass4,
-            hipFuncAttributeMaxDynamicSharedMemorySize, 90112);
-
-        k_pass1<<<1024, 256, 0, stream>>>(feats, (const int*)(ws + PERM_OFF), wt1,
-            A0, C0, b1, Xg, (float*)(ws + P1_OFF), N, nt);
-        k_fin<<<1, TPB, 0, stream>>>((const float*)(ws + P1_OFF), 64, 64, g1, be1, b1,
-                                     A1, C1, fN);
-        k_pass2<<<1024, 256, 0, stream>>>(Xg, wt1, wt2, A1, C1, b2,
-                                          (float*)(ws + P2_OFF), N, nt);
-        k_fin<<<1, TPB, 0, stream>>>((const float*)(ws + P2_OFF), 64, 128, g2, be2, b2,
-                                     A2, C2, fN);
-        k_pass3<<<1024, 512, 65536, stream>>>(Xg, wt1, wt2, wt3, A1, C1, A2, C2, b3,
-                                              (float*)(ws + P3_OFF), N, nt);
+    k_pass1<<<1024, 256, 0, stream>>>(feats, (const int*)(ws + PERM_OFF), wt1,
+        A0, C0, b1, Xg, (float*)(ws + P1_OFF), N, nt);
+    k_fin<<<1, TPB, 0, stream>>>((const float*)(ws + P1_OFF), 64, 64, g1, be1, b1,
+                                 A1, C1, fN);
+
+    k_pass2<<<2048, 256, 0, stream>>>(Xg, wt1, wt2, A1, C1, b2,
+                                      (float*)(ws + P2_OFF), N, nt);
+    k_fin<<<1, TPB, 0, stream>>>((const float*)(ws + P2_OFF), 64, 128, g2, be2, b2,
+                                 A2, C2, fN);
+
+    if (t2) {
+        k_pass3<1><<<1024, 512, 0, stream>>>(Xg, wt1, wt2, wt3, A1, C1, A2, C2, b3,
+                                             (float*)(ws + P3_OFF), H3, N, nt);
         k_fin<<<1, TPB, 0, stream>>>((const float*)(ws + P3_OFF), 64, 256, g3, be3, b3,
                                      A3, C3, fN);
-        k_pass4<<<NVOX / 16, 512, 90112, stream>>>(Xg, wt1, wt2, wt3, wt4,
+        k_pass4l<<<NVOX / 16, 512, 65536, stream>>>(H3, wt4, A3, C3, b4,
+            (const int*)(ws + BASE_OFF), out, N);
+    } else {
+        k_pass3<0><<<1024, 512, 0, stream>>>(Xg, wt1, wt2, wt3, A1, C1, A2, C2, b3,
+                                             (float*)(ws + P3_OFF), H3, N, nt);
+        k_fin<<<1, TPB, 0, stream>>>((const float*)(ws + P3_OFF), 64, 256, g3, be3, b3,
+                                     A3, C3, fN);
+        k_pass4<<<NVOX / 16, 512, 73728, stream>>>(Xg, wt1, wt2, wt3, wt4,
             A1, C1, A2, C2, A3, C3, b4, (const int*)(ws + BASE_OFF), out);
-    } else {
-        const int nblk = (N + PT - 1) / PT;
-        k_stage<1><<<nblk, TPB, SMEM_S1, stream>>>(feats, ws, b1, b2, b3, b4, out, N);
-        k_fin<<<1, TPB, 0, stream>>>((const float*)(ws + P1_OFF), 64, 64, g1, be1, b1,
-                                     (float*)(ws + A1_OFF), (float*)(ws + C1_OFF), fN);
-        k_stage<2><<<nblk, TPB, SMEM_S2, stream>>>(feats, ws, b1, b2, b3, b4, out, N);
-        k_fin<<<1, TPB, 0, stream>>>((const float*)(ws + P2_OFF), 64, 128, g2, be2, b2,
-                                     (float*)(ws + A2_OFF), (float*)(ws + C2_OFF), fN);
-        k_stage<3><<<nblk, TPB, SMEM_S3, stream>>>(feats, ws, b1, b2, b3, b4, out, N);
-        k_fin<<<1, TPB, 0, stream>>>((const float*)(ws + P3_OFF), 64, 256, g3, be3, b3,
-                                     (float*)(ws + A3_OFF), (float*)(ws + C3_OFF), fN);
-        k_stage<4><<<NVOX / VB, TPB, SMEM_S4, stream>>>(feats, ws, b1, b2, b3, b4, out, N);
-    }
-}
+    }
+}
```
